# Performance work log

Measured on AMD Instinct MI355X. Metric: run time of the kernel, lower is better.

Reference implementation:

```python
import jax, jax.numpy as jnp
import numpy as np

N = 50000      # nodes
F_IN = 128     # input features
H = 128        # hidden channels
C = 2          # num classes
E = 1600000    # edges
EPS = 1e-5     # BatchNorm eps


def setup_inputs() -> dict:
    key = jax.random.key(0)
    ks = jax.random.split(key, 4)
    x = jax.random.normal(ks[0], (N, F_IN), dtype=jnp.float32)
    edge_index = jax.random.randint(ks[1], (2, E), 0, N, dtype=jnp.int64)
    W1 = jax.random.normal(ks[2], (F_IN, H), dtype=jnp.float32) * 0.05
    W2 = jax.random.normal(ks[3], (H, C), dtype=jnp.float32) * 0.05
    return {
        "x": x, "edge_index": edge_index,
        "bn0_gamma": jnp.ones((F_IN,), jnp.float32), "bn0_beta": jnp.zeros((F_IN,), jnp.float32),
        "bn0_mean": jnp.zeros((F_IN,), jnp.float32), "bn0_var": jnp.ones((F_IN,), jnp.float32),
        "W1": W1, "b1": jnp.zeros((H,), jnp.float32),
        "bn1_gamma": jnp.ones((H,), jnp.float32), "bn1_beta": jnp.zeros((H,), jnp.float32),
        "bn1_mean": jnp.zeros((H,), jnp.float32), "bn1_var": jnp.ones((H,), jnp.float32),
        "W2": W2, "b2": jnp.zeros((C,), jnp.float32),
    }


def batch_norm_eval(x, gamma, beta, mean, var):
    # BatchNorm over nodes, eval mode: use running stats
    return (x - mean) * jax.lax.rsqrt(var + EPS) * gamma + beta


def gcn_conv(x, edge_index, W, b):
    # GCNConv: x @ W, add self-loops, symmetric deg^{-1/2} normalization, scatter-add
    n = x.shape[0]
    xw = x @ W  # [N, out]
    loop = jnp.arange(n, dtype=edge_index.dtype)
    src = jnp.concatenate([edge_index[0], loop])
    dst = jnp.concatenate([edge_index[1], loop])
    deg = jax.ops.segment_sum(jnp.ones_like(dst, dtype=x.dtype), dst, num_segments=n)
    dinv = jnp.where(deg > 0, jax.lax.rsqrt(jnp.maximum(deg, 1.0)), 0.0)
    norm = dinv[src] * dinv[dst]  # [E+N]
    out = jax.ops.segment_sum(xw[src] * norm[:, None], dst, num_segments=n)
    return out + b


def reference(x, edge_index, bn0_gamma, bn0_beta, bn0_mean, bn0_var,
              W1, b1, bn1_gamma, bn1_beta, bn1_mean, bn1_var, W2, b2):
    # Eval mode: dropout / dropout_edge are identity
    h = batch_norm_eval(x, bn0_gamma, bn0_beta, bn0_mean, bn0_var)
    h = gcn_conv(h, edge_index, W1, b1)
    h = batch_norm_eval(h, bn1_gamma, bn1_beta, bn1_mean, bn1_var)
    h = jax.nn.relu(h)
    return gcn_conv(h, edge_index, W2, b2)
```

## Files before the change

### kernel.cpp

```cpp
#include <hip/hip_runtime.h>

#define EPS 1e-5f
#define CAP 128
#define DR  128
#define NB  391
#define CB  4608
#define GS  16
#define CHUNK 4096
#define GZB ((NB * GS + 255) / 256)

typedef __attribute__((ext_vector_type(8))) short bf16x8;
typedef __attribute__((ext_vector_type(4))) float f32x4;

__device__ __forceinline__ unsigned int f2bf(float f) {
  union { float f; unsigned int u; } v; v.f = f;
  return (v.u + 0x7fffu + ((v.u >> 16) & 1u)) >> 16;
}
__device__ __forceinline__ float bf2f_lo(unsigned int u) {
  union { unsigned int i; float f; } v; v.i = u << 16; return v.f;
}
__device__ __forceinline__ float bf2f_hi(unsigned int u) {
  union { unsigned int i; float f; } v; v.i = u & 0xffff0000u; return v.f;
}

__global__ __launch_bounds__(256) void k_prep_all(
    const float* __restrict__ W1, const float* __restrict__ b1,
    const float* __restrict__ g0, const float* __restrict__ be0,
    const float* __restrict__ m0, const float* __restrict__ v0,
    const float* __restrict__ g1, const float* __restrict__ be1,
    const float* __restrict__ m1, const float* __restrict__ v1,
    const float4* __restrict__ x,
    unsigned short* __restrict__ Wb, float* __restrict__ c1,
    float* __restrict__ s1, float* __restrict__ u1,
    int* __restrict__ gcur, uint2* __restrict__ Xb4, int n4, int npad4) {
  int bid = blockIdx.x;
  int tid = threadIdx.x;
  if (bid == 0) {
    __shared__ float s0s[128], t0s[128];
    if (tid < 128) {
      float s0 = g0[tid] * rsqrtf(v0[tid] + EPS);
      s0s[tid] = s0;
      t0s[tid] = be0[tid] - m0[tid] * s0;
      float s = g1[tid] * rsqrtf(v1[tid] + EPS);
      s1[tid] = s;
      u1[tid] = fmaf(b1[tid] - m1[tid], s, be1[tid]);
    }
    __syncthreads();
    if (tid < 128) {
      float acc = 0.f;
      for (int k = 0; k < 128; ++k) acc = fmaf(t0s[k], W1[k * 128 + tid], acc);
      c1[tid] = acc;
    }
    for (int idx = tid; idx < 16384; idx += 256) {
      int k = idx >> 7, col = idx & 127;
      float w = W1[idx] * s0s[k];
      int c = k >> 5, j = k & 7, lq2 = (k >> 3) & 3;
      int t = col >> 4, li = col & 15;
      Wb[(((c * 8 + t) * 64) + lq2 * 16 + li) * 8 + j] = (unsigned short)f2bf(w);
    }
    return;
  }
  bid -= 1;
  if (bid < GZB) {
    int i = bid * 256 + tid;
    if (i < NB * GS) gcur[i] = 0;
    return;
  }
  bid -= GZB;
  int i = bid * 256 + tid;
  if (i >= npad4) return;
  uint2 o = make_uint2(0u, 0u);
  if (i < n4) {
    float4 v = x[i];
    o.x = (f2bf(v.y) << 16) | f2bf(v.x);
    o.y = (f2bf(v.w) << 16) | f2bf(v.z);
  }
  Xb4[i] = o;
}

__global__ __launch_bounds__(256) void k_p1(const int* __restrict__ esrc,
                                            const int* __restrict__ edst,
                                            int* __restrict__ gcur,
                                            unsigned int* __restrict__ coarse, int e) {
  __shared__ int hist[NB];
  __shared__ int base[NB];
  __shared__ int loff[NB];
  for (int i = threadIdx.x; i < NB; i += 256) { hist[i] = 0; loff[i] = 0; }
  __syncthreads();
  int e0 = blockIdx.x * CHUNK;
  int e1 = min(e0 + CHUNK, e);
  for (int i = e0 + threadIdx.x; i < e1; i += 256)
    atomicAdd(&hist[edst[i] >> 7], 1);
  __syncthreads();
  int rot = blockIdx.x % NB;
  for (int bb = threadIdx.x; bb < NB; bb += 256) {
    int b = bb + rot; if (b >= NB) b -= NB;
    int h = hist[b];
    if (h > 0) base[b] = atomicAdd(&gcur[b * GS], h);
  }
  __syncthreads();
  for (int i = e0 + threadIdx.x; i < e1; i += 256) {
    int d = edst[i], s = esrc[i];
    int b = d >> 7;
    int p = base[b] + atomicAdd(&loff[b], 1);
    if (p < CB) coarse[(size_t)b * CB + p] = ((unsigned int)(d & 127) << 16) | (unsigned int)s;
  }
}

__global__ __launch_bounds__(256) void k_p2(const int* __restrict__ gcur,
                                            const unsigned int* __restrict__ coarse,
                                            unsigned short* __restrict__ slot,
                                            int* __restrict__ wcnt,
                                            float* __restrict__ dinv, int n) {
  __shared__ int lcnt[DR];
  __shared__ int nqr[DR];
  __shared__ unsigned short lslot[DR * CAP];
  for (int i = threadIdx.x; i < DR; i += 256) lcnt[i] = 0;
  unsigned int padpat = ((unsigned int)n << 16) | (unsigned int)n;
  for (int q = threadIdx.x; q < DR * CAP / 2; q += 256) ((unsigned int*)lslot)[q] = padpat;
  __syncthreads();
  int cb = blockIdx.x;
  int cnt = gcur[cb * GS]; if (cnt > CB) cnt = CB;
  const unsigned int* src = coarse + (size_t)cb * CB;
  for (int i = threadIdx.x; i < cnt; i += 256) {
    unsigned int v = src[i];
    int ld = (int)(v >> 16);
    int pos = atomicAdd(&lcnt[ld], 1);
    if (pos < CAP) lslot[ld * CAP + pos] = (unsigned short)(v & 0xffffu);
  }
  __syncthreads();
  int dbase = cb * DR;
  for (int ld = threadIdx.x; ld < DR; ld += 256) {
    int c = min(lcnt[ld], CAP);
    nqr[ld] = ((((c + 3) >> 2) + 3) & ~3);
    int d = dbase + ld;
    if (d < n) {
      wcnt[d] = c;
      dinv[d] = rsqrtf((float)c + 1.0f);
    }
  }
  __syncthreads();
  const uint2* ls8 = (const uint2*)lslot;
  uint2* s8 = (uint2*)slot;
  for (int idx = threadIdx.x; idx < DR * 32; idx += 256) {
    int ld = idx >> 5, qi = idx & 31;
    if (qi < nqr[ld] && dbase + ld < n) s8[(size_t)cb * (DR * 32) + idx] = ls8[idx];
  }
}

__global__ __launch_bounds__(256) void k_gemm1m(const unsigned short* __restrict__ Xb,
                                                const unsigned short* __restrict__ Wb,
                                                const float* __restrict__ c1,
                                                const float* __restrict__ dinv,
                                                unsigned short* __restrict__ xsb, int n) {
  const int tid = threadIdx.x;
  if (blockIdx.x == 0 && tid < 16)
    ((uint4*)xsb)[(size_t)n * 16 + tid] = make_uint4(0, 0, 0, 0);
  const int wave = tid >> 6, lane = tid & 63;
  const int r0 = blockIdx.x * 64 + wave * 16;
  const int lr = lane & 15, lq = lane >> 4;
  const bf16x8* a_base = (const bf16x8*)(Xb + (size_t)(r0 + lr) * 128);
  const bf16x8* wb = (const bf16x8*)Wb;
  f32x4 acc[8];
#pragma unroll
  for (int t = 0; t < 8; ++t) acc[t] = (f32x4){0.f, 0.f, 0.f, 0.f};
#pragma unroll
  for (int c = 0; c < 4; ++c) {
    bf16x8 a = a_base[c * 4 + lq];
#pragma unroll
    for (int t = 0; t < 8; ++t) {
      bf16x8 b = wb[(c * 8 + t) * 64 + lane];
      acc[t] = __builtin_amdgcn_mfma_f32_16x16x32_bf16(a, b, acc[t], 0, 0, 0);
    }
  }
#pragma unroll
  for (int reg = 0; reg < 4; ++reg) {
    int row = r0 + lq * 4 + reg;
    if (row < n) {
      float dd = dinv[row];
      unsigned short* orow = xsb + (size_t)row * 128 + lr;
#pragma unroll
      for (int t = 0; t < 8; ++t) {
        float v = (acc[t][reg] + c1[t * 16 + lr]) * dd;
        orow[t * 16] = (unsigned short)f2bf(v);
      }
    }
  }
}

__global__ __launch_bounds__(256) void k_gather1(const int* __restrict__ wcnt,
                                                 const unsigned short* __restrict__ slot,
                                                 const uint4* __restrict__ xs4,
                                                 const float* __restrict__ dinv,
                                                 const float* __restrict__ s1,
                                                 const float* __restrict__ u1,
                                                 const float* __restrict__ W2,
                                                 float* __restrict__ xs2, int n) {
  int wave = threadIdx.x >> 6, lane = threadIdx.x & 63;
  int d = blockIdx.x * 4 + wave;
  if (d >= n) return;
  int sub = lane >> 4, cl = lane & 15;
  int cnt = wcnt[d];
  int nq4 = ((((cnt + 3) >> 2) + 3) & ~3);
  const unsigned short* slotd = slot + ((size_t)d << 7);
  float a0 = 0.f, a1 = 0.f, a2 = 0.f, a3 = 0.f, a4 = 0.f, a5 = 0.f, a6 = 0.f, a7 = 0.f;
#define ACC(R) { a0 += bf2f_lo(R.x); a1 += bf2f_hi(R.x); a2 += bf2f_lo(R.y); a3 += bf2f_hi(R.y); \
                 a4 += bf2f_lo(R.z); a5 += bf2f_hi(R.z); a6 += bf2f_lo(R.w); a7 += bf2f_hi(R.w); }
  for (int q = 0; q < nq4; q += 4) {
    int i0 = slotd[(q + 0) * 4 + sub];
    int i1 = slotd[(q + 1) * 4 + sub];
    int i2 = slotd[(q + 2) * 4 + sub];
    int i3 = slotd[(q + 3) * 4 + sub];
    uint4 r0 = xs4[(size_t)i0 * 16 + cl];
    uint4 r1 = xs4[(size_t)i1 * 16 + cl];
    uint4 r2 = xs4[(size_t)i2 * 16 + cl];
    uint4 r3 = xs4[(size_t)i3 * 16 + cl];
    ACC(r0); ACC(r1); ACC(r2); ACC(r3);
  }
#define FOLD(OFF) { a0 += __shfl_xor(a0, OFF); a1 += __shfl_xor(a1, OFF); \
                    a2 += __shfl_xor(a2, OFF); a3 += __shfl_xor(a3, OFF); \
                    a4 += __shfl_xor(a4, OFF); a5 += __shfl_xor(a5, OFF); \
                    a6 += __shfl_xor(a6, OFF); a7 += __shfl_xor(a7, OFF); }
  FOLD(16); FOLD(32);
  uint4 sr = xs4[(size_t)d * 16 + cl];
  ACC(sr);
#undef ACC
#undef FOLD
  float dd = dinv[d];
  float4 sA = ((const float4*)s1)[cl * 2], sB = ((const float4*)s1)[cl * 2 + 1];
  float4 uA = ((const float4*)u1)[cl * 2], uB = ((const float4*)u1)[cl * 2 + 1];
  float h0 = fmaxf(fmaf(a0 * dd, sA.x, uA.x), 0.f);
  float h1 = fmaxf(fmaf(a1 * dd, sA.y, uA.y), 0.f);
  float h2 = fmaxf(fmaf(a2 * dd, sA.z, uA.z), 0.f);
  float h3 = fmaxf(fmaf(a3 * dd, sA.w, uA.w), 0.f);
  float h4 = fmaxf(fmaf(a4 * dd, sB.x, uB.x), 0.f);
  float h5 = fmaxf(fmaf(a5 * dd, sB.y, uB.y), 0.f);
  float h6 = fmaxf(fmaf(a6 * dd, sB.z, uB.z), 0.f);
  float h7 = fmaxf(fmaf(a7 * dd, sB.w, uB.w), 0.f);
  float4 wA = ((const float4*)W2)[cl * 4 + 0];
  float4 wB = ((const float4*)W2)[cl * 4 + 1];
  float4 wC = ((const float4*)W2)[cl * 4 + 2];
  float4 wD = ((const float4*)W2)[cl * 4 + 3];
  float p0 = h0 * wA.x + h1 * wA.z + h2 * wB.x + h3 * wB.z
           + h4 * wC.x + h5 * wC.z + h6 * wD.x + h7 * wD.z;
  float p1 = h0 * wA.y + h1 * wA.w + h2 * wB.y + h3 * wB.w
           + h4 * wC.y + h5 * wC.w + h6 * wD.y + h7 * wD.w;
  for (int off = 1; off < 16; off <<= 1) {
    p0 += __shfl_xor(p0, off);
    p1 += __shfl_xor(p1, off);
  }
  if (lane == 0) ((float2*)xs2)[d] = make_float2(p0 * dd, p1 * dd);
}

__global__ __launch_bounds__(256) void k_gather2(const int* __restrict__ wcnt,
                                                 const unsigned short* __restrict__ slot,
                                                 const float* __restrict__ xs2,
                                                 const float* __restrict__ dinv,
                                                 const float* __restrict__ b2,
                                                 float* __restrict__ out, int n) {
  int wave = threadIdx.x >> 6, lane = threadIdx.x & 63;
  int d = blockIdx.x * 4 + wave;
  if (d >= n) return;
  int cnt = wcnt[d];
  const unsigned short* slotd = slot + ((size_t)d << 7);
  float p0 = 0.f, p1 = 0.f;
  for (int k = lane; k < cnt; k += 64) {
    int s = slotd[k];
    float2 v = ((const float2*)xs2)[s];
    p0 += v.x; p1 += v.y;
  }
  for (int off = 32; off > 0; off >>= 1) {
    p0 += __shfl_down(p0, off);
    p1 += __shfl_down(p1, off);
  }
  if (lane == 0) {
    float dd = dinv[d];
    float2 self = ((const float2*)xs2)[d];
    out[d * 2 + 0] = fmaf(dd, p0 + self.x, b2[0]);
    out[d * 2 + 1] = fmaf(dd, p1 + self.y, b2[1]);
  }
}

extern "C" void kernel_launch(void* const* d_in, const int* in_sizes, int n_in,
                              void* d_out, int out_size, void* d_ws, size_t ws_size,
                              hipStream_t stream) {
  const float* x   = (const float*)d_in[0];
  const int*   ei  = (const int*)d_in[1];
  const float* g0  = (const float*)d_in[2];
  const float* be0 = (const float*)d_in[3];
  const float* m0  = (const float*)d_in[4];
  const float* v0  = (const float*)d_in[5];
  const float* W1  = (const float*)d_in[6];
  const float* b1  = (const float*)d_in[7];
  const float* g1  = (const float*)d_in[8];
  const float* be1 = (const float*)d_in[9];
  const float* m1  = (const float*)d_in[10];
  const float* v1  = (const float*)d_in[11];
  const float* W2  = (const float*)d_in[12];
  const float* b2  = (const float*)d_in[13];
  float* out = (float*)d_out;

  const int n = in_sizes[0] / 128;
  const int e = in_sizes[1] / 2;
  const int* esrc = ei;
  const int* edst = ei + e;
  const int npad = ((n + 63) / 64) * 64;

  int*            gcur   = (int*)d_ws;
  unsigned int*   coarse = (unsigned int*)(gcur + 6272);
  unsigned short* slot   = (unsigned short*)(coarse + (size_t)NB * CB);
  int*            wcnt   = (int*)(slot + (size_t)n * CAP);
  float*          dinv   = (float*)(wcnt + n);
  unsigned short* Wb     = (unsigned short*)(dinv + n);
  float*          c1     = (float*)(Wb + 16384);
  float*          s1     = c1 + 128;
  float*          u1     = s1 + 128;
  float*          xs2    = u1 + 128;
  unsigned short* Xb     = (unsigned short*)(xs2 + (size_t)n * 2);
  unsigned short* xsb    = Xb + (size_t)npad * 128;

  const int cvb = (npad * 32 + 255) / 256;
  k_prep_all<<<1 + GZB + cvb, 256, 0, stream>>>(W1, b1, g0, be0, m0, v0, g1, be1, m1, v1,
                                                (const float4*)x, Wb, c1, s1, u1, gcur,
                                                (uint2*)Xb, n * 32, npad * 32);
  k_p1<<<(e + CHUNK - 1) / CHUNK, 256, 0, stream>>>(esrc, edst, gcur, coarse, e);
  k_p2<<<NB, 256, 0, stream>>>(gcur, coarse, slot, wcnt, dinv, n);
  k_gemm1m<<<npad / 64, 256, 0, stream>>>(Xb, Wb, c1, dinv, xsb, n);
  k_gather1<<<(n + 3) / 4, 256, 0, stream>>>(wcnt, slot, (const uint4*)xsb, dinv, s1, u1, W2, xs2, n);
  k_gather2<<<(n + 3) / 4, 256, 0, stream>>>(wcnt, slot, xs2, dinv, b2, out, n);
}
```

Measured before the change: 218.4 us.

## Merge independent stages into shared launches and move source dinv scaling into gather

Merges the edge bucketing pass into the prep kernel, and runs the CSR finalisation alongside the first GEMM in one launch. This is possible because the GEMM no longer multiplies by the source dinv; gather1 now loads dinv per neighbour and applies it with an FMA. The gcur zeroing moves to a hipMemsetAsync, and a zero dinv entry is added for the padding node. The goal is fewer kernel launches and more overlap between independent stages, at the cost of extra dinv gathers in the edge loop.

Measured after the change: 215.1 us. About the same (-1.5%).

```diff
diff --git a/kernel.cpp b/kernel.cpp
--- a/kernel.cpp
+++ b/kernel.cpp
@@ -7,7 +7,6 @@
 #define CB  4608
 #define GS  16
 #define CHUNK 4096
-#define GZB ((NB * GS + 255) / 256)
 
 typedef __attribute__((ext_vector_type(8))) short bf16x8;
 typedef __attribute__((ext_vector_type(4))) float f32x4;
@@ -23,7 +22,9 @@
   union { unsigned int i; float f; } v; v.i = u & 0xffff0000u; return v.f;
 }
 
-__global__ __launch_bounds__(256) void k_prep_all(
+__global__ __launch_bounds__(256) void k_A(
+    const int* __restrict__ esrc, const int* __restrict__ edst,
+    int* __restrict__ gcur, unsigned int* __restrict__ coarse, int e, int nb_p1,
     const float* __restrict__ W1, const float* __restrict__ b1,
     const float* __restrict__ g0, const float* __restrict__ be0,
     const float* __restrict__ m0, const float* __restrict__ v0,
@@ -32,11 +33,38 @@
     const float4* __restrict__ x,
     unsigned short* __restrict__ Wb, float* __restrict__ c1,
     float* __restrict__ s1, float* __restrict__ u1,
-    int* __restrict__ gcur, uint2* __restrict__ Xb4, int n4, int npad4) {
+    float* __restrict__ dinv, unsigned short* __restrict__ xsb,
+    uint2* __restrict__ Xb4, int n, int n4, int npad4) {
+  __shared__ int hist[NB];
+  __shared__ int base[NB];
+  __shared__ int loff[NB];
+  __shared__ float s0s[128], t0s[128];
+  const int tid = threadIdx.x;
   int bid = blockIdx.x;
-  int tid = threadIdx.x;
-  if (bid == 0) {
-    __shared__ float s0s[128], t0s[128];
+  if (bid < nb_p1) {
+    for (int i = tid; i < NB; i += 256) { hist[i] = 0; loff[i] = 0; }
+    __syncthreads();
+    int e0 = bid * CHUNK;
+    int e1 = min(e0 + CHUNK, e);
+    for (int i = e0 + tid; i < e1; i += 256)
+      atomicAdd(&hist[edst[i] >> 7], 1);
+    __syncthreads();
+    int rot = bid % NB;
+    for (int bb = tid; bb < NB; bb += 256) {
+      int b = bb + rot; if (b >= NB) b -= NB;
+      int h = hist[b];
+      if (h > 0) base[b] = atomicAdd(&gcur[b * GS], h);
+    }
+    __syncthreads();
+    for (int i = e0 + tid; i < e1; i += 256) {
+      int d = edst[i], s = esrc[i];
+      int b = d >> 7;
+      int p = base[b] + atomicAdd(&loff[b], 1);
+      if (p < CB) coarse[(size_t)b * CB + p] = ((unsigned int)(d & 127) << 16) | (unsigned int)s;
+    }
+    return;
+  }
+  if (bid == nb_p1) {
     if (tid < 128) {
       float s0 = g0[tid] * rsqrtf(v0[tid] + EPS);
       s0s[tid] = s0;
@@ -51,6 +79,8 @@
       for (int k = 0; k < 128; ++k) acc = fmaf(t0s[k], W1[k * 128 + tid], acc);
       c1[tid] = acc;
     }
+    if (tid == 0) dinv[n] = 0.f;
+    if (tid < 16) ((uint4*)xsb)[(size_t)n * 16 + tid] = make_uint4(0, 0, 0, 0);
     for (int idx = tid; idx < 16384; idx += 256) {
       int k = idx >> 7, col = idx & 127;
       float w = W1[idx] * s0s[k];
@@ -60,14 +90,7 @@
     }
     return;
   }
-  bid -= 1;
-  if (bid < GZB) {
-    int i = bid * 256 + tid;
-    if (i < NB * GS) gcur[i] = 0;
-    return;
-  }
-  bid -= GZB;
-  int i = bid * 256 + tid;
+  int i = (bid - nb_p1 - 1) * 256 + tid;
   if (i >= npad4) return;
   uint2 o = make_uint2(0u, 0u);
   if (i < n4) {
@@ -78,86 +101,52 @@
   Xb4[i] = o;
 }
 
-__global__ __launch_bounds__(256) void k_p1(const int* __restrict__ esrc,
-                                            const int* __restrict__ edst,
-                                            int* __restrict__ gcur,
-                                            unsigned int* __restrict__ coarse, int e) {
-  __shared__ int hist[NB];
-  __shared__ int base[NB];
-  __shared__ int loff[NB];
-  for (int i = threadIdx.x; i < NB; i += 256) { hist[i] = 0; loff[i] = 0; }
-  __syncthreads();
-  int e0 = blockIdx.x * CHUNK;
-  int e1 = min(e0 + CHUNK, e);
-  for (int i = e0 + threadIdx.x; i < e1; i += 256)
-    atomicAdd(&hist[edst[i] >> 7], 1);
-  __syncthreads();
-  int rot = blockIdx.x % NB;
-  for (int bb = threadIdx.x; bb < NB; bb += 256) {
-    int b = bb + rot; if (b >= NB) b -= NB;
-    int h = hist[b];
-    if (h > 0) base[b] = atomicAdd(&gcur[b * GS], h);
-  }
-  __syncthreads();
-  for (int i = e0 + threadIdx.x; i < e1; i += 256) {
-    int d = edst[i], s = esrc[i];
-    int b = d >> 7;
-    int p = base[b] + atomicAdd(&loff[b], 1);
-    if (p < CB) coarse[(size_t)b * CB + p] = ((unsigned int)(d & 127) << 16) | (unsigned int)s;
-  }
-}
-
-__global__ __launch_bounds__(256) void k_p2(const int* __restrict__ gcur,
-                                            const unsigned int* __restrict__ coarse,
-                                            unsigned short* __restrict__ slot,
-                                            int* __restrict__ wcnt,
-                                            float* __restrict__ dinv, int n) {
+__global__ __launch_bounds__(256) void k_B(
+    const int* __restrict__ gcur, const unsigned int* __restrict__ coarse,
+    unsigned short* __restrict__ slot, int* __restrict__ wcnt, float* __restrict__ dinv,
+    const unsigned short* __restrict__ Xb, const unsigned short* __restrict__ Wb,
+    const float* __restrict__ c1, unsigned short* __restrict__ xsb, int n) {
   __shared__ int lcnt[DR];
   __shared__ int nqr[DR];
   __shared__ unsigned short lslot[DR * CAP];
-  for (int i = threadIdx.x; i < DR; i += 256) lcnt[i] = 0;
-  unsigned int padpat = ((unsigned int)n << 16) | (unsigned int)n;
-  for (int q = threadIdx.x; q < DR * CAP / 2; q += 256) ((unsigned int*)lslot)[q] = padpat;
-  __syncthreads();
-  int cb = blockIdx.x;
-  int cnt = gcur[cb * GS]; if (cnt > CB) cnt = CB;
-  const unsigned int* src = coarse + (size_t)cb * CB;
-  for (int i = threadIdx.x; i < cnt; i += 256) {
-    unsigned int v = src[i];
-    int ld = (int)(v >> 16);
-    int pos = atomicAdd(&lcnt[ld], 1);
-    if (pos < CAP) lslot[ld * CAP + pos] = (unsigned short)(v & 0xffffu);
-  }
-  __syncthreads();
-  int dbase = cb * DR;
-  for (int ld = threadIdx.x; ld < DR; ld += 256) {
-    int c = min(lcnt[ld], CAP);
-    nqr[ld] = ((((c + 3) >> 2) + 3) & ~3);
-    int d = dbase + ld;
-    if (d < n) {
-      wcnt[d] = c;
-      dinv[d] = rsqrtf((float)c + 1.0f);
-    }
-  }
-  __syncthreads();
-  const uint2* ls8 = (const uint2*)lslot;
-  uint2* s8 = (uint2*)slot;
-  for (int idx = threadIdx.x; idx < DR * 32; idx += 256) {
-    int ld = idx >> 5, qi = idx & 31;
-    if (qi < nqr[ld] && dbase + ld < n) s8[(size_t)cb * (DR * 32) + idx] = ls8[idx];
-  }
-}
-
-__global__ __launch_bounds__(256) void k_gemm1m(const unsigned short* __restrict__ Xb,
-                                                const unsigned short* __restrict__ Wb,
-                                                const float* __restrict__ c1,
-                                                const float* __restrict__ dinv,
-                                                unsigned short* __restrict__ xsb, int n) {
   const int tid = threadIdx.x;
-  if (blockIdx.x == 0 && tid < 16)
-    ((uint4*)xsb)[(size_t)n * 16 + tid] = make_uint4(0, 0, 0, 0);
+  if (blockIdx.x < NB) {
+    for (int i = tid; i < DR; i += 256) lcnt[i] = 0;
+    unsigned int padpat = ((unsigned int)n << 16) | (unsigned int)n;
+    for (int q = tid; q < DR * CAP / 2; q += 256) ((unsigned int*)lslot)[q] = padpat;
+    __syncthreads();
+    int cb = blockIdx.x;
+    int cnt = gcur[cb * GS]; if (cnt > CB) cnt = CB;
+    const unsigned int* src = coarse + (size_t)cb * CB;
+    for (int i = tid; i < cnt; i += 256) {
+      unsigned int v = src[i];
+      int ld = (int)(v >> 16);
+      int pos = atomicAdd(&lcnt[ld], 1);
+      if (pos < CAP) lslot[ld * CAP + pos] = (unsigned short)(v & 0xffffu);
+    }
+    __syncthreads();
+    int dbase = cb * DR;
+    for (int ld = tid; ld < DR; ld += 256) {
+      int c = min(lcnt[ld], CAP);
+      nqr[ld] = ((((c + 3) >> 2) + 3) & ~3);
+      int d = dbase + ld;
+      if (d < n) {
+        wcnt[d] = c;
+        dinv[d] = rsqrtf((float)c + 1.0f);
+      }
+    }
+    __syncthreads();
+    const uint2* ls8 = (const uint2*)lslot;
+    uint2* s8 = (uint2*)slot;
+    for (int idx = tid; idx < DR * 32; idx += 256) {
+      int ld = idx >> 5, qi = idx & 31;
+      if (qi < nqr[ld] && dbase + ld < n) s8[(size_t)cb * (DR * 32) + idx] = ls8[idx];
+    }
+    return;
+  }
+  const int gb = blockIdx.x - NB;
   const int wave = tid >> 6, lane = tid & 63;
-  const int r0 = blockIdx.x * 64 + wave * 16;
+  const int r0 = gb * 64 + wave * 16;
   const int lr = lane & 15, lq = lane >> 4;
   const bf16x8* a_base = (const bf16x8*)(Xb + (size_t)(r0 + lr) * 128);
   const bf16x8* wb = (const bf16x8*)Wb;
@@ -177,11 +166,10 @@
   for (int reg = 0; reg < 4; ++reg) {
     int row = r0 + lq * 4 + reg;
     if (row < n) {
-      float dd = dinv[row];
       unsigned short* orow = xsb + (size_t)row * 128 + lr;
 #pragma unroll
       for (int t = 0; t < 8; ++t) {
-        float v = (acc[t][reg] + c1[t * 16 + lr]) * dd;
+        float v = acc[t][reg] + c1[t * 16 + lr];
         orow[t * 16] = (unsigned short)f2bf(v);
       }
     }
@@ -204,29 +192,32 @@
   int nq4 = ((((cnt + 3) >> 2) + 3) & ~3);
   const unsigned short* slotd = slot + ((size_t)d << 7);
   float a0 = 0.f, a1 = 0.f, a2 = 0.f, a3 = 0.f, a4 = 0.f, a5 = 0.f, a6 = 0.f, a7 = 0.f;
-#define ACC(R) { a0 += bf2f_lo(R.x); a1 += bf2f_hi(R.x); a2 += bf2f_lo(R.y); a3 += bf2f_hi(R.y); \
-                 a4 += bf2f_lo(R.z); a5 += bf2f_hi(R.z); a6 += bf2f_lo(R.w); a7 += bf2f_hi(R.w); }
+#define ACCF(R, DV) { a0 = fmaf(DV, bf2f_lo(R.x), a0); a1 = fmaf(DV, bf2f_hi(R.x), a1); \
+                      a2 = fmaf(DV, bf2f_lo(R.y), a2); a3 = fmaf(DV, bf2f_hi(R.y), a3); \
+                      a4 = fmaf(DV, bf2f_lo(R.z), a4); a5 = fmaf(DV, bf2f_hi(R.z), a5); \
+                      a6 = fmaf(DV, bf2f_lo(R.w), a6); a7 = fmaf(DV, bf2f_hi(R.w), a7); }
   for (int q = 0; q < nq4; q += 4) {
     int i0 = slotd[(q + 0) * 4 + sub];
     int i1 = slotd[(q + 1) * 4 + sub];
     int i2 = slotd[(q + 2) * 4 + sub];
     int i3 = slotd[(q + 3) * 4 + sub];
+    float d0 = dinv[i0], d1 = dinv[i1], d2 = dinv[i2], d3 = dinv[i3];
     uint4 r0 = xs4[(size_t)i0 * 16 + cl];
     uint4 r1 = xs4[(size_t)i1 * 16 + cl];
     uint4 r2 = xs4[(size_t)i2 * 16 + cl];
     uint4 r3 = xs4[(size_t)i3 * 16 + cl];
-    ACC(r0); ACC(r1); ACC(r2); ACC(r3);
+    ACCF(r0, d0); ACCF(r1, d1); ACCF(r2, d2); ACCF(r3, d3);
   }
 #define FOLD(OFF) { a0 += __shfl_xor(a0, OFF); a1 += __shfl_xor(a1, OFF); \
                     a2 += __shfl_xor(a2, OFF); a3 += __shfl_xor(a3, OFF); \
                     a4 += __shfl_xor(a4, OFF); a5 += __shfl_xor(a5, OFF); \
                     a6 += __shfl_xor(a6, OFF); a7 += __shfl_xor(a7, OFF); }
   FOLD(16); FOLD(32);
+  float dd = dinv[d];
   uint4 sr = xs4[(size_t)d * 16 + cl];
-  ACC(sr);
-#undef ACC
+  ACCF(sr, dd);
+#undef ACCF
 #undef FOLD
-  float dd = dinv[d];
   float4 sA = ((const float4*)s1)[cl * 2], sB = ((const float4*)s1)[cl * 2 + 1];
   float4 uA = ((const float4*)u1)[cl * 2], uB = ((const float4*)u1)[cl * 2 + 1];
   float h0 = fmaxf(fmaf(a0 * dd, sA.x, uA.x), 0.f);
@@ -311,7 +302,7 @@
   unsigned short* slot   = (unsigned short*)(coarse + (size_t)NB * CB);
   int*            wcnt   = (int*)(slot + (size_t)n * CAP);
   float*          dinv   = (float*)(wcnt + n);
-  unsigned short* Wb     = (unsigned short*)(dinv + n);
+  unsigned short* Wb     = (unsigned short*)(dinv + n + 4);
   float*          c1     = (float*)(Wb + 16384);
   float*          s1     = c1 + 128;
   float*          u1     = s1 + 128;
@@ -319,13 +310,14 @@
   unsigned short* Xb     = (unsigned short*)(xs2 + (size_t)n * 2);
   unsigned short* xsb    = Xb + (size_t)npad * 128;
 
-  const int cvb = (npad * 32 + 255) / 256;
-  k_prep_all<<<1 + GZB + cvb, 256, 0, stream>>>(W1, b1, g0, be0, m0, v0, g1, be1, m1, v1,
-                                                (const float4*)x, Wb, c1, s1, u1, gcur,
-                                                (uint2*)Xb, n * 32, npad * 32);
-  k_p1<<<(e + CHUNK - 1) / CHUNK, 256, 0, stream>>>(esrc, edst, gcur, coarse, e);
-  k_p2<<<NB, 256, 0, stream>>>(gcur, coarse, slot, wcnt, dinv, n);
-  k_gemm1m<<<npad / 64, 256, 0, stream>>>(Xb, Wb, c1, dinv, xsb, n);
+  const int nb_p1 = (e + CHUNK - 1) / CHUNK;
+  const int cvb   = (npad * 32 + 255) / 256;
+  hipMemsetAsync(gcur, 0, NB * GS * sizeof(int), stream);
+  k_A<<<nb_p1 + 1 + cvb, 256, 0, stream>>>(esrc, edst, gcur, coarse, e, nb_p1,
+                                           W1, b1, g0, be0, m0, v0, g1, be1, m1, v1,
+                                           (const float4*)x, Wb, c1, s1, u1, dinv, xsb,
+                                           (uint2*)Xb, n, n * 32, npad * 32);
+  k_B<<<NB + npad / 64, 256, 0, stream>>>(gcur, coarse, slot, wcnt, dinv, Xb, Wb, c1, xsb, n);
   k_gather1<<<(n + 3) / 4, 256, 0, stream>>>(wcnt, slot, (const uint4*)xsb, dinv, s1, u1, W2, xs2, n);
   k_gather2<<<(n + 3) / 4, 256, 0, stream>>>(wcnt, slot, xs2, dinv, b2, out, n);
 }
```
